# Optimization experiments

Hardware: AMD Instinct MI355X
Metric: run time of the kernel (lower is better)

## Reference

```python
import jax, jax.numpy as jnp
import numpy as np

NUM_NODES = 100000
IN_DIM = 64
OUT_DIM = 64
NUM_EDGES = 1250000


def setup_inputs() -> dict:
    key = jax.random.key(0)
    k1, k2, k3, k4, k5 = jax.random.split(key, 5)
    x = jax.random.normal(k1, (NUM_NODES, IN_DIM), dtype=jnp.float32)
    edge_index = jax.random.randint(k2, (2, NUM_EDGES), 0, NUM_NODES, dtype=jnp.int32)
    # Linear params (PyTorch default init: uniform(-1/sqrt(in), 1/sqrt(in)))
    bound = 1.0 / np.sqrt(IN_DIM)
    W_self = jax.random.uniform(k3, (OUT_DIM, IN_DIM), minval=-bound, maxval=bound, dtype=jnp.float32)
    b_self = jax.random.uniform(k4, (OUT_DIM,), minval=-bound, maxval=bound, dtype=jnp.float32)
    W_neigh = jax.random.uniform(k5, (OUT_DIM, IN_DIM), minval=-bound, maxval=bound, dtype=jnp.float32)
    return {"x": x, "edge_index": edge_index, "W_self": W_self, "b_self": b_self, "W_neigh": W_neigh}


def reference(x, edge_index, W_self, b_self, W_neigh):
    # x: [N, D_in], edge_index: [2, E]
    src, dst = edge_index[0], edge_index[1]
    num_nodes = x.shape[0]
    x_src = x[src]  # [E, D_in] gather
    neigh_agg = jax.ops.segment_sum(x_src, dst, num_segments=num_nodes)  # [N, D_in]
    deg = jax.ops.segment_sum(jnp.ones_like(dst, dtype=x.dtype), dst, num_segments=num_nodes)
    deg = jnp.clip(deg, 1.0, None)[:, None]
    neigh_mean = neigh_agg / deg
    out = x @ W_self.T + b_self + neigh_mean @ W_neigh.T
    return jax.nn.relu(out)
```

## Files before the change

kernel.cpp:

```cpp
#include <hip/hip_runtime.h>


#define BKSH 9
#define BKN 512
#define NBMAX 256
#define CAPE 7168
#define WPT (CAPE / BKN)
#define CHUNK 4096
#define K1T 512
#define EPT (CHUNK / K1T)

typedef __attribute__((ext_vector_type(8))) short short8;
typedef __attribute__((ext_vector_type(4))) float floatx4;

static __device__ inline unsigned short f2bf(float f) {
  union { float f; unsigned int u; } v;
  v.f = f;
  unsigned int r = v.u + 0x7FFFu + ((v.u >> 16) & 1u);
  return (unsigned short)(r >> 16);
}

static __device__ inline short8 pack8(float4 a, float4 b) {
  short8 s;
  s[0] = (short)f2bf(a.x); s[1] = (short)f2bf(a.y);
  s[2] = (short)f2bf(a.z); s[3] = (short)f2bf(a.w);
  s[4] = (short)f2bf(b.x); s[5] = (short)f2bf(b.y);
  s[6] = (short)f2bf(b.z); s[7] = (short)f2bf(b.w);
  return s;
}

static __device__ inline void add8(float* a, short8 sv) {
  union { short8 s; unsigned int u[4]; } c; c.s = sv;
#pragma unroll
  for (int i = 0; i < 4; ++i) {
    a[2 * i]     += __uint_as_float(c.u[i] << 16);
    a[2 * i + 1] += __uint_as_float(c.u[i] & 0xFFFF0000u);
  }
}

static __device__ inline void cvt8(float* a, short8 sv) {
  union { short8 s; unsigned int u[4]; } c; c.s = sv;
#pragma unroll
  for (int i = 0; i < 4; ++i) {
    a[2 * i]     = __uint_as_float(c.u[i] << 16);
    a[2 * i + 1] = __uint_as_float(c.u[i] & 0xFFFF0000u);
  }
}

__global__ __launch_bounds__(K1T) void k1_main(
    const float* __restrict__ x,
    const float* __restrict__ Wself, const float* __restrict__ bself,
    const float* __restrict__ Wneigh,
    unsigned short* __restrict__ yb, unsigned short* __restrict__ zb,
    const int* __restrict__ src, const int* __restrict__ dst,
    int* __restrict__ cursor, int* __restrict__ ebuf,
    int E, int N, int NB, int SCB) {
  __shared__ int h[NBMAX], loff[NBMAX], gbase[NBMAX];
  __shared__ int sbuf[CHUNK];
  int t = threadIdx.x;
  int bid = blockIdx.x;

  if (bid >= SCB) {
    int lane = t & 63;
    int w = t >> 6;
    int tb = (bid - SCB) * 128 + w * 16;
    int m = lane & 15, q = lane >> 4;

    long long rowA = (long long)min(tb + m, N - 1) * 64;
    short8 ax[2];
#pragma unroll
    for (int ks = 0; ks < 2; ++ks) {
      const float* xr = &x[rowA + ks * 32 + q * 8];
      ax[ks] = pack8(*(const float4*)xr, *(const float4*)(xr + 4));
    }

#pragma unroll
    for (int nt = 0; nt < 4; ++nt) {
      int ob = nt * 16;
      long long rowB = (long long)(ob + m) * 64;
      floatx4 accs = {0.f, 0.f, 0.f, 0.f};
      floatx4 accn = {0.f, 0.f, 0.f, 0.f};
#pragma unroll
      for (int ks = 0; ks < 2; ++ks) {
        const float* pw = &Wself[rowB + ks * 32 + q * 8];
        short8 bs = pack8(*(const float4*)pw, *(const float4*)(pw + 4));
        accs = __builtin_amdgcn_mfma_f32_16x16x32_bf16(ax[ks], bs, accs, 0, 0, 0);
        const float* pn = &Wneigh[rowB + ks * 32 + q * 8];
        short8 bn = pack8(*(const float4*)pn, *(const float4*)(pn + 4));
        accn = __builtin_amdgcn_mfma_f32_16x16x32_bf16(ax[ks], bn, accn, 0, 0, 0);
      }
      float bias = bself[ob + m];
#pragma unroll
      for (int r = 0; r < 4; ++r) {
        int node = tb + q * 4 + r;
        if (node < N) {
          yb[(long long)node * 64 + ob + m] = f2bf(accs[r] + bias);
          zb[(long long)node * 64 + ob + m] = f2bf(accn[r]);
        }
      }
    }
    return;
  }

  int w = t >> 6, lane = t & 63;
  if (t < NBMAX) h[t] = 0;
  __syncthreads();

  int base = bid * CHUNK;
  int myd[EPT], mys[EPT];
#pragma unroll
  for (int i = 0; i < EPT; ++i) {
    int e = base + t + K1T * i;
    if (e < E) {
      myd[i] = dst[e];
      mys[i] = src[e];
      atomicAdd(&h[myd[i] >> BKSH], 1);
    } else myd[i] = -1;
  }
  __syncthreads();

  if (t < 64) {
    int i0 = 4 * t;
    int v0 = h[i0], v1 = h[i0 + 1], v2 = h[i0 + 2], v3 = h[i0 + 3];
    int s4 = v0 + v1 + v2 + v3, inc = s4;
#pragma unroll
    for (int off = 1; off < 64; off <<= 1) {
      int u = __shfl_up(inc, off, 64);
      if (t >= off) inc += u;
    }
    int ex = inc - s4;
    loff[i0] = ex; loff[i0 + 1] = ex + v0;
    loff[i0 + 2] = ex + v0 + v1; loff[i0 + 3] = ex + v0 + v1 + v2;
  }
  __syncthreads();

  if (t < NB) {
    if (h[t] > 0) gbase[t] = t * CAPE + atomicAdd(&cursor[t], h[t]);
  }
  __syncthreads();
  if (t < NBMAX) h[t] = 0;
  __syncthreads();

#pragma unroll
  for (int i = 0; i < EPT; ++i) {
    if (myd[i] >= 0) {
      int b = myd[i] >> BKSH;
      int p = atomicAdd(&h[b], 1);
      sbuf[loff[b] + p] = mys[i] | ((myd[i] & (BKN - 1)) << 17);
    }
  }
  __syncthreads();

  for (int b = w; b < NB; b += 8) {
    int c = h[b], lo = loff[b], go = gbase[b];
    for (int j = lane; j < c; j += 64)
      ebuf[go + j] = sbuf[lo + j];
  }
}

__global__ __launch_bounds__(512) void sb_csr(const int* __restrict__ cursor,
                                              const int* __restrict__ ebuf,
                                              int* __restrict__ col,
                                              int2* __restrict__ rowse, int N) {
  __shared__ int sbuf[CAPE];
  __shared__ int cnt[BKN];
  __shared__ int wsum[8];
  int b = blockIdx.x, t = threadIdx.x;
  int s = b * CAPE;
  int n = cursor[b];
  int e = s + n;

  int my[WPT];
#pragma unroll
  for (int i = 0; i < WPT; ++i) {
    int j = s + t + i * BKN;
    my[i] = (j < e) ? ebuf[j] : -1;
  }

  cnt[t] = 0;
  __syncthreads();
#pragma unroll
  for (int i = 0; i < WPT; ++i)
    if (my[i] >= 0) atomicAdd(&cnt[(my[i] >> 17) & (BKN - 1)], 1);
  __syncthreads();

  int v = cnt[t];
  int lane = t & 63, w = t >> 6;
  int inc = v;
#pragma unroll
  for (int o = 1; o < 64; o <<= 1) {
    int u = __shfl_up(inc, o, 64);
    if (lane >= o) inc += u;
  }
  if (lane == 63) wsum[w] = inc;
  __syncthreads();
  if (t < 8) {
    int s0 = wsum[t], incw = s0;
#pragma unroll
    for (int o = 1; o < 8; o <<= 1) {
      int u = __shfl_up(incw, o, 64);
      if (t >= o) incw += u;
    }
    wsum[t] = incw - s0;
  }
  __syncthreads();
  int ex = wsum[w] + inc - v;
  int node = (b << BKSH) + t;
  if (node < N) rowse[node] = make_int2(s + ex, v);
  __syncthreads();
  cnt[t] = ex;
  __syncthreads();

#pragma unroll
  for (int i = 0; i < WPT; ++i) {
    if (my[i] >= 0) {
      int nl = (my[i] >> 17) & (BKN - 1);
      int p = atomicAdd(&cnt[nl], 1);
      sbuf[p] = my[i] & 0x1FFFF;
    }
  }
  __syncthreads();

  for (int j = t; j < n; j += BKN) col[s + j] = sbuf[j];
}

__global__ __launch_bounds__(256) void gather_final(
    const unsigned short* __restrict__ zb,
    const int2* __restrict__ rowse,
    const int* __restrict__ col,
    const unsigned short* __restrict__ yb,
    float* __restrict__ out, int N) {
  int gid = blockIdx.x * 256 + threadIdx.x;
  int node = gid >> 6;
  if (node >= N) return;
  int lane = threadIdx.x & 63;
  int o = lane >> 3, d = lane & 7;
  int2 se = rowse[node];
  int s = se.x, c = se.y;

  long long ro = (long long)node * 64 + d * 8;
  short8 yv8;
  if (o == 0) {
    yv8 = *(const short8*)&yb[ro];
  }

  float a[8] = {0.f, 0.f, 0.f, 0.f, 0.f, 0.f, 0.f, 0.f};
  float b2[8] = {0.f, 0.f, 0.f, 0.f, 0.f, 0.f, 0.f, 0.f};
  if (c > 0 && c <= 64) {
    int colv = col[s + min(lane, c - 1)];
    for (int kb = 0; kb < c; kb += 16) {
      int k0 = kb + o;
      int k1 = k0 + 8;
      bool p0 = k0 < c, p1 = k1 < c;
      int c0 = __shfl(colv, p0 ? k0 : 0, 64);
      int c1 = __shfl(colv, p1 ? k1 : 0, 64);
      short8 v0 = *(const short8*)&zb[(long long)c0 * 64 + d * 8];
      short8 v1 = *(const short8*)&zb[(long long)c1 * 64 + d * 8];
      if (p0) add8(a, v0);
      if (p1) add8(b2, v1);
    }
  } else if (c > 64) {
    int e = s + c;
    for (int j = s + o; j < e; j += 16) {
      int c0 = col[j];
      bool h2 = (j + 8) < e;
      int c1 = h2 ? col[j + 8] : c0;
      short8 v0 = *(const short8*)&zb[(long long)c0 * 64 + d * 8];
      short8 v1 = *(const short8*)&zb[(long long)c1 * 64 + d * 8];
      add8(a, v0);
      if (h2) add8(b2, v1);
    }
  }
#pragma unroll
  for (int k = 0; k < 8; ++k) a[k] += b2[k];

#pragma unroll
  for (int m = 8; m <= 32; m <<= 1) {
#pragma unroll
    for (int k = 0; k < 8; ++k) a[k] += __shfl_xor(a[k], m, 64);
  }

  if (o == 0) {
    float inv = 1.0f / fmaxf((float)c, 1.0f);
    float yv[8];
    cvt8(yv, yv8);
    float4 r0, r1;
    r0.x = fmaxf(yv[0] + a[0] * inv, 0.f);
    r0.y = fmaxf(yv[1] + a[1] * inv, 0.f);
    r0.z = fmaxf(yv[2] + a[2] * inv, 0.f);
    r0.w = fmaxf(yv[3] + a[3] * inv, 0.f);
    r1.x = fmaxf(yv[4] + a[4] * inv, 0.f);
    r1.y = fmaxf(yv[5] + a[5] * inv, 0.f);
    r1.z = fmaxf(yv[6] + a[6] * inv, 0.f);
    r1.w = fmaxf(yv[7] + a[7] * inv, 0.f);
    *(float4*)&out[ro] = r0;
    *(float4*)&out[ro + 4] = r1;
  }
}

extern "C" void kernel_launch(void* const* d_in, const int* in_sizes, int n_in,
                              void* d_out, int out_size, void* d_ws, size_t ws_size,
                              hipStream_t stream) {
  const float* x      = (const float*)d_in[0];
  const int*   eidx   = (const int*)d_in[1];
  const float* Wself  = (const float*)d_in[2];
  const float* bself  = (const float*)d_in[3];
  const float* Wneigh = (const float*)d_in[4];
  float* out = (float*)d_out;

  const int N = in_sizes[0] / 64;
  const int E = in_sizes[1] / 2;
  const int* src = eidx;
  const int* dst = eidx + E;
  const int NB = (N + BKN - 1) / BKN;

  unsigned short* yb = (unsigned short*)d_ws;
  unsigned short* zb = yb + (size_t)N * 64;
  int* cursor = (int*)(zb + (size_t)N * 64);
  int2* rowse = (int2*)(cursor + NBMAX);
  int* ebuf   = (int*)(rowse + N);
  int* col    = ebuf + (size_t)NB * CAPE;

  hipMemsetAsync(cursor, 0, NBMAX * sizeof(int), stream);

  const int SCB = (E + CHUNK - 1) / CHUNK;
  const int GB = (N + 127) / 128;
  k1_main<<<SCB + GB, K1T, 0, stream>>>(x, Wself, bself, Wneigh, yb, zb,
                                        src, dst, cursor, ebuf, E, N, NB, SCB);
  sb_csr<<<NB, BKN, 0, stream>>>(cursor, ebuf, col, rowse, N);
  gather_final<<<(int)(((long long)N * 64 + 255) / 256), 256, 0, stream>>>(
      zb, rowse, col, yb, out, N);
}
```

Measured before the change: 164.6 us.

## Split edge bucketing into count, scan and scatter kernels for deterministic placement

The fused binning kernel is replaced by three passes. The first pass builds per-chunk bucket histograms, fused with the GEMM, which now uses 256-thread blocks. A scan kernel then computes per-chunk global offsets for each bucket, and a scatter kernel writes the edges. This removes the global atomicAdd on the bucket cursors and the memset, and makes edge order within each bucket deterministic. In exchange it adds two kernel launches, reads dst twice, and writes and reads the counts and base arrays.

```diff
diff --git a/kernel.cpp b/kernel.cpp
--- a/kernel.cpp
+++ b/kernel.cpp
@@ -7,8 +7,7 @@
 #define CAPE 7168
 #define WPT (CAPE / BKN)
 #define CHUNK 4096
-#define K1T 512
-#define EPT (CHUNK / K1T)
+#define EPT (CHUNK / 256)
 
 typedef __attribute__((ext_vector_type(8))) short short8;
 typedef __attribute__((ext_vector_type(4))) float floatx4;
@@ -47,23 +46,21 @@
   }
 }
 
-__global__ __launch_bounds__(K1T) void k1_main(
+__global__ __launch_bounds__(256) void k_count_gemm(
     const float* __restrict__ x,
     const float* __restrict__ Wself, const float* __restrict__ bself,
     const float* __restrict__ Wneigh,
     unsigned short* __restrict__ yb, unsigned short* __restrict__ zb,
-    const int* __restrict__ src, const int* __restrict__ dst,
-    int* __restrict__ cursor, int* __restrict__ ebuf,
-    int E, int N, int NB, int SCB) {
-  __shared__ int h[NBMAX], loff[NBMAX], gbase[NBMAX];
-  __shared__ int sbuf[CHUNK];
+    const int* __restrict__ dst, int* __restrict__ counts,
+    int E, int N, int SCB) {
+  __shared__ int h[NBMAX];
   int t = threadIdx.x;
   int bid = blockIdx.x;
 
   if (bid >= SCB) {
     int lane = t & 63;
     int w = t >> 6;
-    int tb = (bid - SCB) * 128 + w * 16;
+    int tb = (bid - SCB) * 64 + w * 16;
     int m = lane & 15, q = lane >> 4;
 
     long long rowA = (long long)min(tb + m, N - 1) * 64;
@@ -102,15 +99,66 @@
     return;
   }
 
+  if (t < NBMAX) h[t] = 0;
+  __syncthreads();
+  int base = bid * CHUNK;
+#pragma unroll
+  for (int i = 0; i < EPT; ++i) {
+    int e = base + t + 256 * i;
+    if (e < E) atomicAdd(&h[dst[e] >> BKSH], 1);
+  }
+  __syncthreads();
+  if (t < NBMAX) counts[bid * NBMAX + t] = h[t];
+}
+
+__global__ __launch_bounds__(512) void k_scan(const int* __restrict__ counts,
+                                              int* __restrict__ base,
+                                              int* __restrict__ cursor, int SCB) {
+  __shared__ int wsum[8];
+  int b = blockIdx.x, t = threadIdx.x;
+  int v = (t < SCB) ? counts[t * NBMAX + b] : 0;
+
+  int lane = t & 63, w = t >> 6;
+  int inc = v;
+#pragma unroll
+  for (int o = 1; o < 64; o <<= 1) {
+    int u = __shfl_up(inc, o, 64);
+    if (lane >= o) inc += u;
+  }
+  if (lane == 63) wsum[w] = inc;
+  __syncthreads();
+  if (t < 8) {
+    int s0 = wsum[t], incw = s0;
+#pragma unroll
+    for (int o = 1; o < 8; o <<= 1) {
+      int u = __shfl_up(incw, o, 64);
+      if (t >= o) incw += u;
+    }
+    wsum[t] = incw - s0;
+  }
+  __syncthreads();
+  int ex = wsum[w] + inc - v;
+  if (t < SCB) base[t * NBMAX + b] = b * CAPE + ex;
+  if (t == 511) cursor[b] = ex + v;
+}
+
+__global__ __launch_bounds__(256) void k_scatter(
+    const int* __restrict__ src, const int* __restrict__ dst,
+    const int* __restrict__ base, int* __restrict__ ebuf, int E, int NB) {
+  __shared__ int h[NBMAX], loff[NBMAX], gbase[NBMAX];
+  __shared__ int sbuf[CHUNK];
+  int t = threadIdx.x;
+  int bid = blockIdx.x;
   int w = t >> 6, lane = t & 63;
+
   if (t < NBMAX) h[t] = 0;
   __syncthreads();
 
-  int base = bid * CHUNK;
+  int eb = bid * CHUNK;
   int myd[EPT], mys[EPT];
 #pragma unroll
   for (int i = 0; i < EPT; ++i) {
-    int e = base + t + K1T * i;
+    int e = eb + t + 256 * i;
     if (e < E) {
       myd[i] = dst[e];
       mys[i] = src[e];
@@ -132,11 +180,7 @@
     loff[i0] = ex; loff[i0 + 1] = ex + v0;
     loff[i0 + 2] = ex + v0 + v1; loff[i0 + 3] = ex + v0 + v1 + v2;
   }
-  __syncthreads();
-
-  if (t < NB) {
-    if (h[t] > 0) gbase[t] = t * CAPE + atomicAdd(&cursor[t], h[t]);
-  }
+  if (t < NBMAX) gbase[t] = base[bid * NBMAX + t];
   __syncthreads();
   if (t < NBMAX) h[t] = 0;
   __syncthreads();
@@ -151,7 +195,7 @@
   }
   __syncthreads();
 
-  for (int b = w; b < NB; b += 8) {
+  for (int b = w; b < NB; b += 4) {
     int c = h[b], lo = loff[b], go = gbase[b];
     for (int j = lane; j < c; j += 64)
       ebuf[go + j] = sbuf[lo + j];
@@ -313,20 +357,22 @@
   const int* src = eidx;
   const int* dst = eidx + E;
   const int NB = (N + BKN - 1) / BKN;
+  const int SCB = (E + CHUNK - 1) / CHUNK;
 
   unsigned short* yb = (unsigned short*)d_ws;
   unsigned short* zb = yb + (size_t)N * 64;
   int* cursor = (int*)(zb + (size_t)N * 64);
   int2* rowse = (int2*)(cursor + NBMAX);
-  int* ebuf   = (int*)(rowse + N);
+  int* counts = (int*)(rowse + N);
+  int* basep  = counts + (size_t)SCB * NBMAX;
+  int* ebuf   = basep + (size_t)SCB * NBMAX;
   int* col    = ebuf + (size_t)NB * CAPE;
 
-  hipMemsetAsync(cursor, 0, NBMAX * sizeof(int), stream);
-
-  const int SCB = (E + CHUNK - 1) / CHUNK;
-  const int GB = (N + 127) / 128;
-  k1_main<<<SCB + GB, K1T, 0, stream>>>(x, Wself, bself, Wneigh, yb, zb,
-                                        src, dst, cursor, ebuf, E, N, NB, SCB);
+  const int GB = (N + 63) / 64;
+  k_count_gemm<<<SCB + GB, 256, 0, stream>>>(x, Wself, bself, Wneigh, yb, zb,
+                                             dst, counts, E, N, SCB);
+  k_scan<<<NB, 512, 0, stream>>>(counts, basep, cursor, SCB);
+  k_scatter<<<SCB, 256, 0, stream>>>(src, dst, basep, ebuf, E, NB);
   sb_csr<<<NB, BKN, 0, stream>>>(cursor, ebuf, col, rowse, N);
   gather_final<<<(int)(((long long)N * 64 + 255) / 256), 256, 0, stream>>>(
       zb, rowse, col, yb, out, N);
```

Measured after the change: 177.2 us. +7.6%, slower.

## Fuse CSR bucket sort with neighbor gather and shrink edge-scatter blocks

Applied to the files above, without the earlier changes.

Merges the per-bucket CSR build and the gather/epilogue into one 1024-thread kernel. Column indices now stay in shared memory, so the col and rowse arrays are no longer written and read back through global memory, and one launch disappears. Each wave then walks 32 nodes serially using the shared-memory offsets. The first kernel also drops to 256 threads per block, covering 64 nodes in its GEMM part and 16 edges per thread in its scatter part. The trade-off is that the gather now runs on only one block per 512-node bucket, which cuts the number of concurrent waves available to hide random-access latency.

```diff
diff --git a/kernel.cpp b/kernel.cpp
--- a/kernel.cpp
+++ b/kernel.cpp
@@ -5,10 +5,9 @@
 #define BKN 512
 #define NBMAX 256
 #define CAPE 7168
-#define WPT (CAPE / BKN)
 #define CHUNK 4096
-#define K1T 512
-#define EPT (CHUNK / K1T)
+#define EPT (CHUNK / 256)
+#define WPT2 (CAPE / 1024)
 
 typedef __attribute__((ext_vector_type(8))) short short8;
 typedef __attribute__((ext_vector_type(4))) float floatx4;
@@ -47,7 +46,7 @@
   }
 }
 
-__global__ __launch_bounds__(K1T) void k1_main(
+__global__ __launch_bounds__(256) void k1_main(
     const float* __restrict__ x,
     const float* __restrict__ Wself, const float* __restrict__ bself,
     const float* __restrict__ Wneigh,
@@ -63,7 +62,7 @@
   if (bid >= SCB) {
     int lane = t & 63;
     int w = t >> 6;
-    int tb = (bid - SCB) * 128 + w * 16;
+    int tb = (bid - SCB) * 64 + w * 16;
     int m = lane & 15, q = lane >> 4;
 
     long long rowA = (long long)min(tb + m, N - 1) * 64;
@@ -110,7 +109,7 @@
   int myd[EPT], mys[EPT];
 #pragma unroll
   for (int i = 0; i < EPT; ++i) {
-    int e = base + t + K1T * i;
+    int e = base + t + 256 * i;
     if (e < E) {
       myd[i] = dst[e];
       mys[i] = src[e];
@@ -151,48 +150,53 @@
   }
   __syncthreads();
 
-  for (int b = w; b < NB; b += 8) {
+  for (int b = w; b < NB; b += 4) {
     int c = h[b], lo = loff[b], go = gbase[b];
     for (int j = lane; j < c; j += 64)
       ebuf[go + j] = sbuf[lo + j];
   }
 }
 
-__global__ __launch_bounds__(512) void sb_csr(const int* __restrict__ cursor,
-                                              const int* __restrict__ ebuf,
-                                              int* __restrict__ col,
-                                              int2* __restrict__ rowse, int N) {
+__global__ __launch_bounds__(1024) void sb_gather(
+    const int* __restrict__ cursor,
+    const int* __restrict__ ebuf,
+    const unsigned short* __restrict__ zb,
+    const unsigned short* __restrict__ yb,
+    float* __restrict__ out, int N) {
   __shared__ int sbuf[CAPE];
   __shared__ int cnt[BKN];
+  __shared__ int off[BKN];
   __shared__ int wsum[8];
   int b = blockIdx.x, t = threadIdx.x;
   int s = b * CAPE;
   int n = cursor[b];
   int e = s + n;
 
-  int my[WPT];
-#pragma unroll
-  for (int i = 0; i < WPT; ++i) {
-    int j = s + t + i * BKN;
+  int my[WPT2];
+#pragma unroll
+  for (int i = 0; i < WPT2; ++i) {
+    int j = s + t + (i << 10);
     my[i] = (j < e) ? ebuf[j] : -1;
   }
-
-  cnt[t] = 0;
-  __syncthreads();
-#pragma unroll
-  for (int i = 0; i < WPT; ++i)
+  if (t < BKN) cnt[t] = 0;
+  __syncthreads();
+#pragma unroll
+  for (int i = 0; i < WPT2; ++i)
     if (my[i] >= 0) atomicAdd(&cnt[(my[i] >> 17) & (BKN - 1)], 1);
   __syncthreads();
 
-  int v = cnt[t];
+  int v = 0, inc = 0;
   int lane = t & 63, w = t >> 6;
-  int inc = v;
-#pragma unroll
-  for (int o = 1; o < 64; o <<= 1) {
-    int u = __shfl_up(inc, o, 64);
-    if (lane >= o) inc += u;
-  }
-  if (lane == 63) wsum[w] = inc;
+  if (t < BKN) {
+    v = cnt[t];
+    inc = v;
+#pragma unroll
+    for (int o = 1; o < 64; o <<= 1) {
+      int u = __shfl_up(inc, o, 64);
+      if (lane >= o) inc += u;
+    }
+    if (lane == 63) wsum[w] = inc;
+  }
   __syncthreads();
   if (t < 8) {
     int s0 = wsum[t], incw = s0;
@@ -204,15 +208,15 @@
     wsum[t] = incw - s0;
   }
   __syncthreads();
-  int ex = wsum[w] + inc - v;
-  int node = (b << BKSH) + t;
-  if (node < N) rowse[node] = make_int2(s + ex, v);
-  __syncthreads();
-  cnt[t] = ex;
-  __syncthreads();
-
-#pragma unroll
-  for (int i = 0; i < WPT; ++i) {
+  if (t < BKN) {
+    int ex = wsum[w] + inc - v;
+    off[t] = ex;
+    cnt[t] = ex;
+  }
+  __syncthreads();
+
+#pragma unroll
+  for (int i = 0; i < WPT2; ++i) {
     if (my[i] >= 0) {
       int nl = (my[i] >> 17) & (BKN - 1);
       int p = atomicAdd(&cnt[nl], 1);
@@ -221,80 +225,55 @@
   }
   __syncthreads();
 
-  for (int j = t; j < n; j += BKN) col[s + j] = sbuf[j];
-}
-
-__global__ __launch_bounds__(256) void gather_final(
-    const unsigned short* __restrict__ zb,
-    const int2* __restrict__ rowse,
-    const int* __restrict__ col,
-    const unsigned short* __restrict__ yb,
-    float* __restrict__ out, int N) {
-  int gid = blockIdx.x * 256 + threadIdx.x;
-  int node = gid >> 6;
-  if (node >= N) return;
-  int lane = threadIdx.x & 63;
   int o = lane >> 3, d = lane & 7;
-  int2 se = rowse[node];
-  int s = se.x, c = se.y;
-
-  long long ro = (long long)node * 64 + d * 8;
-  short8 yv8;
-  if (o == 0) {
-    yv8 = *(const short8*)&yb[ro];
-  }
-
-  float a[8] = {0.f, 0.f, 0.f, 0.f, 0.f, 0.f, 0.f, 0.f};
-  float b2[8] = {0.f, 0.f, 0.f, 0.f, 0.f, 0.f, 0.f, 0.f};
-  if (c > 0 && c <= 64) {
-    int colv = col[s + min(lane, c - 1)];
+  int nl0 = w * 32;
+  for (int nl = nl0; nl < nl0 + 32; ++nl) {
+    int node = (b << BKSH) + nl;
+    if (node >= N) break;
+    int s0 = off[nl];
+    int c = cnt[nl] - s0;
+
+    long long ro = (long long)node * 64 + d * 8;
+    short8 yv8;
+    if (o == 0) yv8 = *(const short8*)&yb[ro];
+
+    float a[8] = {0.f, 0.f, 0.f, 0.f, 0.f, 0.f, 0.f, 0.f};
+    float b2[8] = {0.f, 0.f, 0.f, 0.f, 0.f, 0.f, 0.f, 0.f};
     for (int kb = 0; kb < c; kb += 16) {
-      int k0 = kb + o;
-      int k1 = k0 + 8;
+      int k0 = kb + o, k1 = k0 + 8;
       bool p0 = k0 < c, p1 = k1 < c;
-      int c0 = __shfl(colv, p0 ? k0 : 0, 64);
-      int c1 = __shfl(colv, p1 ? k1 : 0, 64);
+      int c0 = sbuf[s0 + (p0 ? k0 : 0)];
+      int c1 = sbuf[s0 + (p1 ? k1 : 0)];
       short8 v0 = *(const short8*)&zb[(long long)c0 * 64 + d * 8];
       short8 v1 = *(const short8*)&zb[(long long)c1 * 64 + d * 8];
       if (p0) add8(a, v0);
       if (p1) add8(b2, v1);
     }
-  } else if (c > 64) {
-    int e = s + c;
-    for (int j = s + o; j < e; j += 16) {
-      int c0 = col[j];
-      bool h2 = (j + 8) < e;
-      int c1 = h2 ? col[j + 8] : c0;
-      short8 v0 = *(const short8*)&zb[(long long)c0 * 64 + d * 8];
-      short8 v1 = *(const short8*)&zb[(long long)c1 * 64 + d * 8];
-      add8(a, v0);
-      if (h2) add8(b2, v1);
-    }
-  }
-#pragma unroll
-  for (int k = 0; k < 8; ++k) a[k] += b2[k];
-
-#pragma unroll
-  for (int m = 8; m <= 32; m <<= 1) {
-#pragma unroll
-    for (int k = 0; k < 8; ++k) a[k] += __shfl_xor(a[k], m, 64);
-  }
-
-  if (o == 0) {
-    float inv = 1.0f / fmaxf((float)c, 1.0f);
-    float yv[8];
-    cvt8(yv, yv8);
-    float4 r0, r1;
-    r0.x = fmaxf(yv[0] + a[0] * inv, 0.f);
-    r0.y = fmaxf(yv[1] + a[1] * inv, 0.f);
-    r0.z = fmaxf(yv[2] + a[2] * inv, 0.f);
-    r0.w = fmaxf(yv[3] + a[3] * inv, 0.f);
-    r1.x = fmaxf(yv[4] + a[4] * inv, 0.f);
-    r1.y = fmaxf(yv[5] + a[5] * inv, 0.f);
-    r1.z = fmaxf(yv[6] + a[6] * inv, 0.f);
-    r1.w = fmaxf(yv[7] + a[7] * inv, 0.f);
-    *(float4*)&out[ro] = r0;
-    *(float4*)&out[ro + 4] = r1;
+#pragma unroll
+    for (int k = 0; k < 8; ++k) a[k] += b2[k];
+
+#pragma unroll
+    for (int m = 8; m <= 32; m <<= 1) {
+#pragma unroll
+      for (int k = 0; k < 8; ++k) a[k] += __shfl_xor(a[k], m, 64);
+    }
+
+    if (o == 0) {
+      float inv = 1.0f / fmaxf((float)c, 1.0f);
+      float yv[8];
+      cvt8(yv, yv8);
+      float4 r0, r1;
+      r0.x = fmaxf(yv[0] + a[0] * inv, 0.f);
+      r0.y = fmaxf(yv[1] + a[1] * inv, 0.f);
+      r0.z = fmaxf(yv[2] + a[2] * inv, 0.f);
+      r0.w = fmaxf(yv[3] + a[3] * inv, 0.f);
+      r1.x = fmaxf(yv[4] + a[4] * inv, 0.f);
+      r1.y = fmaxf(yv[5] + a[5] * inv, 0.f);
+      r1.z = fmaxf(yv[6] + a[6] * inv, 0.f);
+      r1.w = fmaxf(yv[7] + a[7] * inv, 0.f);
+      *(float4*)&out[ro] = r0;
+      *(float4*)&out[ro + 4] = r1;
+    }
   }
 }
 
@@ -313,21 +292,17 @@
   const int* src = eidx;
   const int* dst = eidx + E;
   const int NB = (N + BKN - 1) / BKN;
+  const int SCB = (E + CHUNK - 1) / CHUNK;
 
   unsigned short* yb = (unsigned short*)d_ws;
   unsigned short* zb = yb + (size_t)N * 64;
   int* cursor = (int*)(zb + (size_t)N * 64);
-  int2* rowse = (int2*)(cursor + NBMAX);
-  int* ebuf   = (int*)(rowse + N);
-  int* col    = ebuf + (size_t)NB * CAPE;
+  int* ebuf   = cursor + NBMAX;
 
   hipMemsetAsync(cursor, 0, NBMAX * sizeof(int), stream);
 
-  const int SCB = (E + CHUNK - 1) / CHUNK;
-  const int GB = (N + 127) / 128;
-  k1_main<<<SCB + GB, K1T, 0, stream>>>(x, Wself, bself, Wneigh, yb, zb,
+  const int GB = (N + 63) / 64;
+  k1_main<<<SCB + GB, 256, 0, stream>>>(x, Wself, bself, Wneigh, yb, zb,
                                         src, dst, cursor, ebuf, E, N, NB, SCB);
-  sb_csr<<<NB, BKN, 0, stream>>>(cursor, ebuf, col, rowse, N);
-  gather_final<<<(int)(((long long)N * 64 + 255) / 256), 256, 0, stream>>>(
-      zb, rowse, col, yb, out, N);
-}
+  sb_gather<<<NB, 1024, 0, stream>>>(cursor, ebuf, zb, yb, out, N);
+}
```

After: 177.7 us. 1.08x slower.

## Map eight nodes per wavefront in gather and halve k1 block size

Applied to the files above, without the earlier changes.

The gather kernel now gives each 8-lane group of a wavefront its own node, instead of spreading one node's edges across the whole wavefront. Each lane loads column indices in chunks of 8 and broadcasts them with shuffles, so the cross-lane shuffle reduction at the end disappears and all lanes write output. The wavefront loops to the largest degree among its 8 nodes, so nodes with uneven degrees cause some idle iterations. Separately, k1_main drops from 512 to 256 threads per block, which changes edges per thread and rows per GEMM block and doubles the number of GEMM blocks.

```diff
diff --git a/kernel.cpp b/kernel.cpp
--- a/kernel.cpp
+++ b/kernel.cpp
@@ -7,8 +7,7 @@
 #define CAPE 7168
 #define WPT (CAPE / BKN)
 #define CHUNK 4096
-#define K1T 512
-#define EPT (CHUNK / K1T)
+#define EPT (CHUNK / 256)
 
 typedef __attribute__((ext_vector_type(8))) short short8;
 typedef __attribute__((ext_vector_type(4))) float floatx4;
@@ -47,7 +46,7 @@
   }
 }
 
-__global__ __launch_bounds__(K1T) void k1_main(
+__global__ __launch_bounds__(256) void k1_main(
     const float* __restrict__ x,
     const float* __restrict__ Wself, const float* __restrict__ bself,
     const float* __restrict__ Wneigh,
@@ -63,7 +62,7 @@
   if (bid >= SCB) {
     int lane = t & 63;
     int w = t >> 6;
-    int tb = (bid - SCB) * 128 + w * 16;
+    int tb = (bid - SCB) * 64 + w * 16;
     int m = lane & 15, q = lane >> 4;
 
     long long rowA = (long long)min(tb + m, N - 1) * 64;
@@ -110,7 +109,7 @@
   int myd[EPT], mys[EPT];
 #pragma unroll
   for (int i = 0; i < EPT; ++i) {
-    int e = base + t + K1T * i;
+    int e = base + t + 256 * i;
     if (e < E) {
       myd[i] = dst[e];
       mys[i] = src[e];
@@ -151,7 +150,7 @@
   }
   __syncthreads();
 
-  for (int b = w; b < NB; b += 8) {
+  for (int b = w; b < NB; b += 4) {
     int c = h[b], lo = loff[b], go = gbase[b];
     for (int j = lane; j < c; j += 64)
       ebuf[go + j] = sbuf[lo + j];
@@ -224,63 +223,47 @@
   for (int j = t; j < n; j += BKN) col[s + j] = sbuf[j];
 }
 
-__global__ __launch_bounds__(256) void gather_final(
+__global__ __launch_bounds__(256) void gather_oct(
     const unsigned short* __restrict__ zb,
     const int2* __restrict__ rowse,
     const int* __restrict__ col,
     const unsigned short* __restrict__ yb,
     float* __restrict__ out, int N) {
-  int gid = blockIdx.x * 256 + threadIdx.x;
-  int node = gid >> 6;
-  if (node >= N) return;
-  int lane = threadIdx.x & 63;
+  int t = threadIdx.x;
+  int lane = t & 63, w = t >> 6;
   int o = lane >> 3, d = lane & 7;
-  int2 se = rowse[node];
-  int s = se.x, c = se.y;
+  int node = blockIdx.x * 32 + w * 8 + o;
+
+  int2 se = rowse[min(node, N - 1)];
+  int s0 = se.x;
+  int c = (node < N) ? se.y : 0;
+  int cm1 = max(c - 1, 0);
+
+  int cmax = c;
+#pragma unroll
+  for (int m = 8; m <= 32; m <<= 1) cmax = max(cmax, __shfl_xor(cmax, m, 64));
 
   long long ro = (long long)node * 64 + d * 8;
-  short8 yv8;
-  if (o == 0) {
-    yv8 = *(const short8*)&yb[ro];
-  }
+  long long ros = (long long)min(node, N - 1) * 64 + d * 8;
+  short8 yv8 = *(const short8*)&yb[ros];
 
   float a[8] = {0.f, 0.f, 0.f, 0.f, 0.f, 0.f, 0.f, 0.f};
   float b2[8] = {0.f, 0.f, 0.f, 0.f, 0.f, 0.f, 0.f, 0.f};
-  if (c > 0 && c <= 64) {
-    int colv = col[s + min(lane, c - 1)];
-    for (int kb = 0; kb < c; kb += 16) {
-      int k0 = kb + o;
-      int k1 = k0 + 8;
-      bool p0 = k0 < c, p1 = k1 < c;
-      int c0 = __shfl(colv, p0 ? k0 : 0, 64);
-      int c1 = __shfl(colv, p1 ? k1 : 0, 64);
-      short8 v0 = *(const short8*)&zb[(long long)c0 * 64 + d * 8];
-      short8 v1 = *(const short8*)&zb[(long long)c1 * 64 + d * 8];
-      if (p0) add8(a, v0);
-      if (p1) add8(b2, v1);
-    }
-  } else if (c > 64) {
-    int e = s + c;
-    for (int j = s + o; j < e; j += 16) {
-      int c0 = col[j];
-      bool h2 = (j + 8) < e;
-      int c1 = h2 ? col[j + 8] : c0;
-      short8 v0 = *(const short8*)&zb[(long long)c0 * 64 + d * 8];
-      short8 v1 = *(const short8*)&zb[(long long)c1 * 64 + d * 8];
-      add8(a, v0);
-      if (h2) add8(b2, v1);
+  for (int kb = 0; kb < cmax; kb += 8) {
+    int colv = col[s0 + min(kb + d, cm1)];
+#pragma unroll
+    for (int j = 0; j < 8; ++j) {
+      bool p = (kb + j) < c;
+      int cs = __shfl(colv, (lane & 56) | j, 64);
+      cs = p ? cs : 0;
+      short8 v = *(const short8*)&zb[(long long)cs * 64 + d * 8];
+      if (p) add8((j & 1) ? b2 : a, v);
     }
   }
 #pragma unroll
   for (int k = 0; k < 8; ++k) a[k] += b2[k];
 
-#pragma unroll
-  for (int m = 8; m <= 32; m <<= 1) {
-#pragma unroll
-    for (int k = 0; k < 8; ++k) a[k] += __shfl_xor(a[k], m, 64);
-  }
-
-  if (o == 0) {
+  if (node < N) {
     float inv = 1.0f / fmaxf((float)c, 1.0f);
     float yv[8];
     cvt8(yv, yv8);
@@ -313,6 +296,7 @@
   const int* src = eidx;
   const int* dst = eidx + E;
   const int NB = (N + BKN - 1) / BKN;
+  const int SCB = (E + CHUNK - 1) / CHUNK;
 
   unsigned short* yb = (unsigned short*)d_ws;
   unsigned short* zb = yb + (size_t)N * 64;
@@ -323,11 +307,9 @@
 
   hipMemsetAsync(cursor, 0, NBMAX * sizeof(int), stream);
 
-  const int SCB = (E + CHUNK - 1) / CHUNK;
-  const int GB = (N + 127) / 128;
-  k1_main<<<SCB + GB, K1T, 0, stream>>>(x, Wself, bself, Wneigh, yb, zb,
+  const int GB = (N + 63) / 64;
+  k1_main<<<SCB + GB, 256, 0, stream>>>(x, Wself, bself, Wneigh, yb, zb,
                                         src, dst, cursor, ebuf, E, N, NB, SCB);
   sb_csr<<<NB, BKN, 0, stream>>>(cursor, ebuf, col, rowse, N);
-  gather_final<<<(int)(((long long)N * 64 + 255) / 256), 256, 0, stream>>>(
-      zb, rowse, col, yb, out, N);
-}
+  gather_oct<<<(N + 31) / 32, 256, 0, stream>>>(zb, rowse, col, yb, out, N);
+}
```

Result: faster. 156.7 us (-4.8%).
